# Optimization experiments

Measured on AMD Instinct MI355X. Metric: run time of the kernel, lower is better.

Reference implementation:

```python
import jax, jax.numpy as jnp
import numpy as np

N = 100_000
E = 1_600_000
D_IN, D_H, D_L = 128, 64, 32


def _glorot(key, shape):
    fan_in, fan_out = shape[0], shape[1]
    s = jnp.sqrt(6.0 / (fan_in + fan_out)).astype(jnp.float32)
    return jax.random.uniform(key, shape, jnp.float32, -s, s)


def setup_inputs() -> dict:
    key = jax.random.key(0)
    ks = jax.random.split(key, 8)
    x = jax.random.normal(ks[0], (N, D_IN), jnp.float32)
    edge_index = jax.random.randint(ks[1], (2, E), 0, N, dtype=jnp.int64)
    return {
        "x": x,
        "edge_index": edge_index,
        "W1": _glorot(ks[2], (D_IN, D_H)),
        "b1": jnp.zeros((D_H,), jnp.float32),
        "W2": _glorot(ks[3], (D_H, D_L)),
        "b2": jnp.zeros((D_L,), jnp.float32),
        "Wd1": _glorot(ks[4], (D_L, D_H)),
        "bd1": jnp.zeros((D_H,), jnp.float32),
        "Wd2": _glorot(ks[5], (D_H, D_IN)),
        "bd2": jnp.zeros((D_IN,), jnp.float32),
    }


def gcn_conv(x, W, b, src, dst, num_nodes):
    """PyG GCNConv: add self-loops, symmetric normalization, aggregate, bias."""
    loop = jnp.arange(num_nodes, dtype=src.dtype)
    s = jnp.concatenate([src, loop])  # sources (message senders)
    d = jnp.concatenate([dst, loop])  # targets (message receivers)
    deg = jax.ops.segment_sum(jnp.ones_like(s, dtype=x.dtype), d, num_segments=num_nodes)
    dinv = jnp.where(deg > 0, jax.lax.rsqrt(deg), 0.0)
    norm = dinv[s] * dinv[d]                      # [E+N]
    h = x @ W                                     # [N, out] dense transform first
    msgs = h[s] * norm[:, None]                   # gather + scale, [E+N, out]
    out = jax.ops.segment_sum(msgs, d, num_segments=num_nodes)  # scatter-add
    return out + b


def reference(x, edge_index, W1, b1, W2, b2, Wd1, bd1, Wd2, bd2):
    src, dst = edge_index[0], edge_index[1]
    n = x.shape[0]
    z = gcn_conv(x, W1, b1, src, dst, n)
    z = jax.nn.relu(z)
    z = gcn_conv(z, W2, b2, src, dst, n)          # latent embedding
    h = jax.nn.relu(z @ Wd1 + bd1)
    reconstructed_x = h @ Wd2 + bd2
    return (reconstructed_x, z)
```

## Files before the change

### kernel.cpp

```cpp
#include <hip/hip_runtime.h>
#include <stdint.h>

#define N_NODES 100000
#define N_EDGES 1600000
#define D_INF   128
#define D_HID   64
#define D_LAT   32
#define NB      98

typedef __attribute__((ext_vector_type(8))) short bf16x8;
typedef __attribute__((ext_vector_type(4))) float f32x4;
typedef __attribute__((ext_vector_type(8))) unsigned short u16x8;

__device__ __forceinline__ unsigned short f2bf(float v) {
  union { float f; unsigned int u; } x; x.f = v;
  unsigned int u = x.u + 0x7FFF + ((x.u >> 16) & 1);
  return (unsigned short)(u >> 16);
}
__device__ __forceinline__ float bf2f(unsigned short h) {
  union { unsigned int u; float f; } x; x.u = ((unsigned int)h) << 16;
  return x.f;
}


#define NBKT      196
#define BKT_SHIFT 9
#define BKT_CAP   10240
#define EPB       4096
#define ABLOCKS   391
#define SPLITB    4
#define SPLITC    4

__global__ void k_zeroinit(int* __restrict__ counts, int* __restrict__ bkcnt) {
  int i = blockIdx.x * 256 + threadIdx.x;
  if (i < N_NODES) counts[i] = 0;
  if (blockIdx.x == 0 && threadIdx.x < NBKT) bkcnt[threadIdx.x] = 0;
}

__global__ __launch_bounds__(256) void k_binA(const int* __restrict__ esrc,
                                              const int* __restrict__ edst,
                                              int* __restrict__ bkcnt,
                                              int2* __restrict__ stage) {
  __shared__ int cnt[NBKT];
  __shared__ int sc[256];
  __shared__ int garel[NBKT];
  __shared__ int pos[NBKT];
  __shared__ __align__(16) int2 stg[EPB];
  __shared__ int gaddr[EPB];
  int t = threadIdx.x;
  int e0 = blockIdx.x * EPB;

  for (int i = t; i < NBKT; i += 256) cnt[i] = 0;
  __syncthreads();

  int ds[16], ss[16];
  const int4* s4 = (const int4*)esrc;
  const int4* d4 = (const int4*)edst;
#pragma unroll
  for (int i = 0; i < 4; i++) {
    int idx4 = (e0 >> 2) + i * 256 + t;
    int4 dd = make_int4(-1, -1, -1, -1);
    int4 sv = make_int4(0, 0, 0, 0);
    if (idx4 < N_EDGES / 4) { dd = d4[idx4]; sv = s4[idx4]; }
    ds[i*4+0] = dd.x; ds[i*4+1] = dd.y; ds[i*4+2] = dd.z; ds[i*4+3] = dd.w;
    ss[i*4+0] = sv.x; ss[i*4+1] = sv.y; ss[i*4+2] = sv.z; ss[i*4+3] = sv.w;
  }
#pragma unroll
  for (int j = 0; j < 16; j++)
    if (ds[j] >= 0) atomicAdd(&cnt[ds[j] >> BKT_SHIFT], 1);
  __syncthreads();

  int c = (t < NBKT) ? cnt[t] : 0;
  sc[t] = c;
  __syncthreads();
  int incl = c;
#pragma unroll
  for (int off = 1; off < 256; off <<= 1) {
    int x = (t >= off) ? sc[t - off] : 0;
    __syncthreads();
    incl += x;
    sc[t] = incl;
    __syncthreads();
  }
  if (t < NBKT) {
    int lb = incl - c;
    int gb = 0;
    if (c > 0) gb = t * BKT_CAP + atomicAdd(&bkcnt[t], c);
    garel[t] = gb - lb;
    pos[t]   = lb;
  }
  __syncthreads();

#pragma unroll
  for (int j = 0; j < 16; j++) {
    if (ds[j] >= 0) {
      int b  = ds[j] >> BKT_SHIFT;
      int lp = atomicAdd(&pos[b], 1);
      stg[lp]   = make_int2(ss[j], ds[j]);
      gaddr[lp] = garel[b] + lp;
    }
  }
  __syncthreads();

  int nval = N_EDGES - e0; if (nval > EPB) nval = EPB;
  for (int i = t; i < nval; i += 256)
    stage[gaddr[i]] = stg[i];
}

__global__ __launch_bounds__(256) void k_countB(const int2* __restrict__ stage,
                                                const int* __restrict__ bkcnt,
                                                int* __restrict__ counts) {
  __shared__ int hist[1 << BKT_SHIFT];
  int b   = blockIdx.x / SPLITC;
  int sub = blockIdx.x % SPLITC;
  int t = threadIdx.x;
  for (int i = t; i < (1 << BKT_SHIFT); i += 256) hist[i] = 0;
  __syncthreads();
  int n = bkcnt[b];
  int nlo = b << BKT_SHIFT;
  const int2* reg = stage + (size_t)b * BKT_CAP;
  for (int i = sub * 256 + t; i < n; i += SPLITC * 256)
    atomicAdd(&hist[reg[i].y - nlo], 1);
  __syncthreads();
  for (int i = t; i < (1 << BKT_SHIFT); i += 256) {
    int node = nlo + i;
    if (node < N_NODES) {
      int v = hist[i];
      if (v) atomicAdd(&counts[node], v);
    }
  }
}

__global__ void k_blocksum(const int* __restrict__ counts, int* __restrict__ bsums) {
  __shared__ int red[4];
  int base = blockIdx.x * 1024 + threadIdx.x * 4;
  int s = 0;
#pragma unroll
  for (int j = 0; j < 4; j++) { int i = base + j; if (i < N_NODES) s += counts[i]; }
#pragma unroll
  for (int off = 32; off > 0; off >>= 1) s += __shfl_down(s, off, 64);
  if ((threadIdx.x & 63) == 0) red[threadIdx.x >> 6] = s;
  __syncthreads();
  if (threadIdx.x == 0) bsums[blockIdx.x] = red[0] + red[1] + red[2] + red[3];
}

__global__ void k_scanblocks(const int* __restrict__ bsums, int* __restrict__ bbase,
                             int* __restrict__ offsets) {
  __shared__ int sh[128];
  int t = threadIdx.x;
  int v = (t < NB) ? bsums[t] : 0;
  sh[t] = v;
  __syncthreads();
  int incl = v;
#pragma unroll
  for (int off = 1; off < 128; off <<= 1) {
    int x = (t >= off) ? sh[t - off] : 0;
    __syncthreads();
    incl += x;
    sh[t] = incl;
    __syncthreads();
  }
  if (t < NB) bbase[t] = incl - v;
  if (t == NB - 1) offsets[N_NODES] = incl;
}

__global__ void k_scanchunk(const int* __restrict__ counts, const int* __restrict__ bbase,
                            int* __restrict__ offsets, int* __restrict__ cursor,
                            float* __restrict__ dinv) {
  __shared__ int sh[256];
  int b = blockIdx.x, t = threadIdx.x;
  int base = b * 1024 + t * 4;
  int v[4]; int s = 0;
#pragma unroll
  for (int j = 0; j < 4; j++) { v[j] = (base + j < N_NODES) ? counts[base + j] : 0; s += v[j]; }
  sh[t] = s;
  __syncthreads();
  int incl = s;
#pragma unroll
  for (int off = 1; off < 256; off <<= 1) {
    int x = (t >= off) ? sh[t - off] : 0;
    __syncthreads();
    incl += x;
    sh[t] = incl;
    __syncthreads();
  }
  int run = bbase[b] + incl - s;
#pragma unroll
  for (int j = 0; j < 4; j++) {
    int i = base + j;
    if (i < N_NODES) {
      offsets[i] = run;
      cursor[i]  = run;
      dinv[i]    = rsqrtf((float)(v[j] + 1));
      run += v[j];
    }
  }
}

__global__ __launch_bounds__(256) void k_binB(const int2* __restrict__ stage,
                                              const int* __restrict__ bkcnt,
                                              int* __restrict__ cursor,
                                              const float* __restrict__ dinv,
                                              int2* __restrict__ csr8) {
  int b   = blockIdx.x / SPLITB;
  int sub = blockIdx.x % SPLITB;
  int n = bkcnt[b];
  const int2* reg = stage + (size_t)b * BKT_CAP;
  for (int i = sub * 256 + threadIdx.x; i < n; i += SPLITB * 256) {
    int2 e = reg[i];
    int slot = atomicAdd(&cursor[e.y], 1);
    float w = dinv[e.x] * dinv[e.y];
    csr8[slot] = make_int2(e.x, __float_as_int(w));
  }
}


__global__ void k_prep_w(const float* __restrict__ W1, const float* __restrict__ W2,
                         const float* __restrict__ Wd1, const float* __restrict__ Wd2,
                         unsigned short* __restrict__ w1hi, unsigned short* __restrict__ w1lo,
                         unsigned short* __restrict__ w2hi, unsigned short* __restrict__ w2lo,
                         unsigned short* __restrict__ wd1hi, unsigned short* __restrict__ wd1lo,
                         unsigned short* __restrict__ wd2hi, unsigned short* __restrict__ wd2lo) {
  const float* src; unsigned short *hi, *lo; int K, M;
  switch (blockIdx.x) {
    case 0:  src = W1;  hi = w1hi;  lo = w1lo;  K = 128; M = 64;  break;
    case 1:  src = W2;  hi = w2hi;  lo = w2lo;  K = 64;  M = 32;  break;
    case 2:  src = Wd1; hi = wd1hi; lo = wd1lo; K = 32;  M = 64;  break;
    default: src = Wd2; hi = wd2hi; lo = wd2lo; K = 64;  M = 128; break;
  }
  int KP = K + 8;
  for (int i = threadIdx.x; i < K * M; i += 256) {
    int k = i / M, c = i % M;
    float v = src[i];
    unsigned short h = f2bf(v);
    hi[c * KP + k] = h;
    lo[c * KP + k] = f2bf(v - bf2f(h));
  }
}


template<int NODES, int K, int M>
__global__ __launch_bounds__(256) void k_mfma_gemm(const float* __restrict__ X,
                                                   const unsigned short* __restrict__ Bhi,
                                                   const unsigned short* __restrict__ Blo,
                                                   unsigned short* __restrict__ Y16) {
  constexpr int KP     = K + 8;
  constexpr int NSTRIP = M / 16;
  constexpr int KSTEPS = K / 32;
  constexpr int MTW    = (NODES / 16) * NSTRIP / 4;
  __shared__ __align__(16) unsigned short Ahi[NODES * KP];
  __shared__ __align__(16) unsigned short Alo[NODES * KP];

  int t = threadIdx.x;
  int node0 = blockIdx.x * NODES;

  for (int i = t; i < NODES * K / 4; i += 256) {
    int n = i / (K / 4), f4 = i % (K / 4);
    float4 v = make_float4(0.f, 0.f, 0.f, 0.f);
    if (node0 + n < N_NODES) v = ((const float4*)(X + (size_t)(node0 + n) * K))[f4];
    int base = n * KP + f4 * 4;
    float vv[4] = {v.x, v.y, v.z, v.w};
#pragma unroll
    for (int j = 0; j < 4; j++) {
      unsigned short h = f2bf(vv[j]);
      Ahi[base + j] = h;
      Alo[base + j] = f2bf(vv[j] - bf2f(h));
    }
  }
  __syncthreads();

  int w = t >> 6, lane = t & 63;
  int quad = lane >> 4, r16 = lane & 15;
  int strip = w % NSTRIP;

  bf16x8 bh[KSTEPS], bl[KSTEPS];
  const unsigned short* bp = Bhi + (strip * 16 + r16) * KP + quad * 8;
  const unsigned short* bq = Blo + (strip * 16 + r16) * KP + quad * 8;
#pragma unroll
  for (int ks = 0; ks < KSTEPS; ks++) {
    bh[ks] = *(const bf16x8*)(bp + ks * 32);
    bl[ks] = *(const bf16x8*)(bq + ks * 32);
  }

#pragma unroll
  for (int c = 0; c < MTW; c++) {
    int mt = (w / NSTRIP) * MTW + c;
    f32x4 acc = {0.f, 0.f, 0.f, 0.f};
    const unsigned short* ap = &Ahi[(mt * 16 + r16) * KP + quad * 8];
    const unsigned short* aq = &Alo[(mt * 16 + r16) * KP + quad * 8];
#pragma unroll
    for (int ks = 0; ks < KSTEPS; ks++) {
      bf16x8 ah = *(const bf16x8*)(ap + ks * 32);
      bf16x8 al = *(const bf16x8*)(aq + ks * 32);
      acc = __builtin_amdgcn_mfma_f32_16x16x32_bf16(ah, bh[ks], acc, 0, 0, 0);
      acc = __builtin_amdgcn_mfma_f32_16x16x32_bf16(ah, bl[ks], acc, 0, 0, 0);
      acc = __builtin_amdgcn_mfma_f32_16x16x32_bf16(al, bh[ks], acc, 0, 0, 0);
    }
    int gn  = node0 + mt * 16 + quad * 4;
    int col = strip * 16 + r16;
#pragma unroll
    for (int r = 0; r < 4; r++) {
      if (gn + r < N_NODES) Y16[(size_t)(gn + r) * M + col] = f2bf(acc[r]);
    }
  }
}


template<int FEAT, bool RELU>
__global__ __launch_bounds__(256) void k_aggregate(const unsigned short* __restrict__ H16,
                            const int* __restrict__ offsets,
                            const int2* __restrict__ csr8,
                            const float* __restrict__ dinv, const float* __restrict__ bias,
                            float* __restrict__ OUT) {
  constexpr int LPE    = FEAT / 8;
  constexpr int GROUPS = 64 / LPE;

  int node = blockIdx.x * 4 + (threadIdx.x >> 6);
  int lane = threadIdx.x & 63;
  if (node >= N_NODES) return;
  int beg = offsets[node], end = offsets[node + 1];
  int g  = lane / LPE;
  int f8 = lane % LPE;

  float a0=0.f,a1=0.f,a2=0.f,a3=0.f,a4=0.f,a5=0.f,a6=0.f,a7=0.f;

  for (int p = beg; p < end; p += 2 * GROUPS) {
    int q0 = p + g, q1 = p + GROUPS + g;
    int2 e0 = (q0 < end) ? csr8[q0] : make_int2(node, 0);
    int2 e1 = (q1 < end) ? csr8[q1] : make_int2(node, 0);
    u16x8 h0 = *(const u16x8*)(H16 + (size_t)e0.x * FEAT + f8 * 8);
    u16x8 h1 = *(const u16x8*)(H16 + (size_t)e1.x * FEAT + f8 * 8);
    float w0 = __int_as_float(e0.y), w1 = __int_as_float(e1.y);
    a0 += bf2f(h0[0]) * w0; a1 += bf2f(h0[1]) * w0;
    a2 += bf2f(h0[2]) * w0; a3 += bf2f(h0[3]) * w0;
    a4 += bf2f(h0[4]) * w0; a5 += bf2f(h0[5]) * w0;
    a6 += bf2f(h0[6]) * w0; a7 += bf2f(h0[7]) * w0;
    a0 += bf2f(h1[0]) * w1; a1 += bf2f(h1[1]) * w1;
    a2 += bf2f(h1[2]) * w1; a3 += bf2f(h1[3]) * w1;
    a4 += bf2f(h1[4]) * w1; a5 += bf2f(h1[5]) * w1;
    a6 += bf2f(h1[6]) * w1; a7 += bf2f(h1[7]) * w1;
  }

#pragma unroll
  for (int off = LPE; off < 64; off <<= 1) {
    a0 += __shfl_xor(a0, off, 64);
    a1 += __shfl_xor(a1, off, 64);
    a2 += __shfl_xor(a2, off, 64);
    a3 += __shfl_xor(a3, off, 64);
    a4 += __shfl_xor(a4, off, 64);
    a5 += __shfl_xor(a5, off, 64);
    a6 += __shfl_xor(a6, off, 64);
    a7 += __shfl_xor(a7, off, 64);
  }

  if (g == 0) {
    float di = dinv[node];
    float sw = di * di;
    u16x8 hs = *(const u16x8*)(H16 + (size_t)node * FEAT + f8 * 8);
    float4 bv0 = *(const float4*)(bias + f8 * 8);
    float4 bv1 = *(const float4*)(bias + f8 * 8 + 4);
    a0 += bf2f(hs[0]) * sw + bv0.x;
    a1 += bf2f(hs[1]) * sw + bv0.y;
    a2 += bf2f(hs[2]) * sw + bv0.z;
    a3 += bf2f(hs[3]) * sw + bv0.w;
    a4 += bf2f(hs[4]) * sw + bv1.x;
    a5 += bf2f(hs[5]) * sw + bv1.y;
    a6 += bf2f(hs[6]) * sw + bv1.z;
    a7 += bf2f(hs[7]) * sw + bv1.w;
    if (RELU) {
      a0 = fmaxf(a0, 0.f); a1 = fmaxf(a1, 0.f);
      a2 = fmaxf(a2, 0.f); a3 = fmaxf(a3, 0.f);
      a4 = fmaxf(a4, 0.f); a5 = fmaxf(a5, 0.f);
      a6 = fmaxf(a6, 0.f); a7 = fmaxf(a7, 0.f);
    }
    float4 o0; o0.x = a0; o0.y = a1; o0.z = a2; o0.w = a3;
    float4 o1; o1.x = a4; o1.y = a5; o1.z = a6; o1.w = a7;
    *(float4*)(OUT + (size_t)node * FEAT + f8 * 8)     = o0;
    *(float4*)(OUT + (size_t)node * FEAT + f8 * 8 + 4) = o1;
  }
}


__global__ __launch_bounds__(256) void k_decoder_mfma(
    const float* __restrict__ Z,
    const unsigned short* __restrict__ B1hi, const unsigned short* __restrict__ B1lo,
    const float* __restrict__ bd1,
    const unsigned short* __restrict__ B2hi, const unsigned short* __restrict__ B2lo,
    const float* __restrict__ bd2, float* __restrict__ RECON) {
  constexpr int KP1 = 40;
  constexpr int KP2 = 72;
  __shared__ __align__(16) unsigned short Azhi[64 * KP1];
  __shared__ __align__(16) unsigned short Azlo[64 * KP1];
  __shared__ __align__(16) unsigned short H3hi[64 * KP2];
  __shared__ __align__(16) unsigned short H3lo[64 * KP2];
  int t = threadIdx.x;
  int node0 = blockIdx.x * 64;

  for (int i = t; i < 512; i += 256) {
    int n = i >> 3, f4 = i & 7;
    float4 v = make_float4(0.f, 0.f, 0.f, 0.f);
    if (node0 + n < N_NODES) v = ((const float4*)(Z + (size_t)(node0 + n) * 32))[f4];
    int base = n * KP1 + f4 * 4;
    float vv[4] = {v.x, v.y, v.z, v.w};
#pragma unroll
    for (int j = 0; j < 4; j++) {
      unsigned short h = f2bf(vv[j]);
      Azhi[base + j] = h;
      Azlo[base + j] = f2bf(vv[j] - bf2f(h));
    }
  }
  __syncthreads();

  int w = t >> 6, lane = t & 63;
  int quad = lane >> 4, r16 = lane & 15;

  {
    int col = w * 16 + r16;
    float bias1 = bd1[col];
    bf16x8 bh = *(const bf16x8*)(B1hi + col * KP1 + quad * 8);
    bf16x8 bl = *(const bf16x8*)(B1lo + col * KP1 + quad * 8);
#pragma unroll
    for (int m = 0; m < 4; m++) {
      bf16x8 ah = *(const bf16x8*)(Azhi + (m * 16 + r16) * KP1 + quad * 8);
      bf16x8 al = *(const bf16x8*)(Azlo + (m * 16 + r16) * KP1 + quad * 8);
      f32x4 acc = {0.f, 0.f, 0.f, 0.f};
      acc = __builtin_amdgcn_mfma_f32_16x16x32_bf16(ah, bh, acc, 0, 0, 0);
      acc = __builtin_amdgcn_mfma_f32_16x16x32_bf16(ah, bl, acc, 0, 0, 0);
      acc = __builtin_amdgcn_mfma_f32_16x16x32_bf16(al, bh, acc, 0, 0, 0);
#pragma unroll
      for (int r = 0; r < 4; r++) {
        int row = m * 16 + quad * 4 + r;
        float hv = fmaxf(acc[r] + bias1, 0.f);
        unsigned short h = f2bf(hv);
        H3hi[row * KP2 + col] = h;
        H3lo[row * KP2 + col] = f2bf(hv - bf2f(h));
      }
    }
  }
  __syncthreads();

#pragma unroll
  for (int sp = 0; sp < 2; sp++) {
    int strip = w + sp * 4;
    int col = strip * 16 + r16;
    float bias2 = bd2[col];
    const unsigned short* b2h = B2hi + col * KP2 + quad * 8;
    const unsigned short* b2l = B2lo + col * KP2 + quad * 8;
    bf16x8 bh0 = *(const bf16x8*)(b2h);
    bf16x8 bh1 = *(const bf16x8*)(b2h + 32);
    bf16x8 bl0 = *(const bf16x8*)(b2l);
    bf16x8 bl1 = *(const bf16x8*)(b2l + 32);
#pragma unroll
    for (int m = 0; m < 4; m++) {
      const unsigned short* ahp = H3hi + (m * 16 + r16) * KP2 + quad * 8;
      const unsigned short* alp = H3lo + (m * 16 + r16) * KP2 + quad * 8;
      bf16x8 ah0 = *(const bf16x8*)(ahp);
      bf16x8 ah1 = *(const bf16x8*)(ahp + 32);
      bf16x8 al0 = *(const bf16x8*)(alp);
      bf16x8 al1 = *(const bf16x8*)(alp + 32);
      f32x4 acc = {0.f, 0.f, 0.f, 0.f};
      acc = __builtin_amdgcn_mfma_f32_16x16x32_bf16(ah0, bh0, acc, 0, 0, 0);
      acc = __builtin_amdgcn_mfma_f32_16x16x32_bf16(ah1, bh1, acc, 0, 0, 0);
      acc = __builtin_amdgcn_mfma_f32_16x16x32_bf16(ah0, bl0, acc, 0, 0, 0);
      acc = __builtin_amdgcn_mfma_f32_16x16x32_bf16(ah1, bl1, acc, 0, 0, 0);
      acc = __builtin_amdgcn_mfma_f32_16x16x32_bf16(al0, bh0, acc, 0, 0, 0);
      acc = __builtin_amdgcn_mfma_f32_16x16x32_bf16(al1, bh1, acc, 0, 0, 0);
#pragma unroll
      for (int r = 0; r < 4; r++) {
        int n = node0 + m * 16 + quad * 4 + r;
        if (n < N_NODES) RECON[(size_t)n * 128 + col] = acc[r] + bias2;
      }
    }
  }
}


extern "C" void kernel_launch(void* const* d_in, const int* in_sizes, int n_in,
                              void* d_out, int out_size, void* d_ws, size_t ws_size,
                              hipStream_t stream) {
  const float* x    = (const float*)d_in[0];
  const int*   eidx = (const int*)d_in[1];
  const int*   esrc = eidx;
  const int*   edst = eidx + N_EDGES;
  const float* W1  = (const float*)d_in[2];
  const float* b1  = (const float*)d_in[3];
  const float* W2  = (const float*)d_in[4];
  const float* b2  = (const float*)d_in[5];
  const float* Wd1 = (const float*)d_in[6];
  const float* bd1 = (const float*)d_in[7];
  const float* Wd2 = (const float*)d_in[8];
  const float* bd2 = (const float*)d_in[9];

  float* recon = (float*)d_out;
  float* z     = (float*)d_out + (size_t)N_NODES * D_INF;
  int2*           stage = (int2*)recon;
  unsigned short* h1_16 = (unsigned short*)recon;
  float*          z1    = (float*)((char*)recon + 12800000);
  unsigned short* h2_16 = (unsigned short*)((char*)recon + 38400000);

  char* ws = (char*)d_ws;
  int*   counts  = (int*)(ws + 0);
  int*   offsets = (int*)(ws + 409600);
  int*   cursor  = (int*)(ws + 819200);
  float* dinv    = (float*)(ws + 1228800);
  int*   bsums   = (int*)(ws + 1638400);
  int*   bbase   = (int*)(ws + 1639424);
  int2*  csr8    = (int2*)(ws + 1640448);
  unsigned short* w1hi  = (unsigned short*)(ws + 14440448);
  unsigned short* w1lo  = (unsigned short*)(ws + 14457856);
  unsigned short* w2hi  = (unsigned short*)(ws + 14475264);
  unsigned short* w2lo  = (unsigned short*)(ws + 14479872);
  unsigned short* wd1hi = (unsigned short*)(ws + 14484480);
  unsigned short* wd1lo = (unsigned short*)(ws + 14489600);
  unsigned short* wd2hi = (unsigned short*)(ws + 14494720);
  unsigned short* wd2lo = (unsigned short*)(ws + 14513152);
  int*   bkcnt  = (int*)(ws + 14531584);

  k_zeroinit<<<391, 256, 0, stream>>>(counts, bkcnt);
  k_binA<<<ABLOCKS, 256, 0, stream>>>(esrc, edst, bkcnt, stage);
  k_countB<<<NBKT * SPLITC, 256, 0, stream>>>(stage, bkcnt, counts);
  k_blocksum<<<NB, 256, 0, stream>>>(counts, bsums);
  k_scanblocks<<<1, 128, 0, stream>>>(bsums, bbase, offsets);
  k_scanchunk<<<NB, 256, 0, stream>>>(counts, bbase, offsets, cursor, dinv);
  k_binB<<<NBKT * SPLITB, 256, 0, stream>>>(stage, bkcnt, cursor, dinv, csr8);
  k_prep_w<<<4, 256, 0, stream>>>(W1, W2, Wd1, Wd2, w1hi, w1lo, w2hi, w2lo,
                                  wd1hi, wd1lo, wd2hi, wd2lo);

  k_mfma_gemm<64, 128, 64><<<(N_NODES + 63) / 64, 256, 0, stream>>>(x, w1hi, w1lo, h1_16);
  k_aggregate<64, true><<<(N_NODES + 3) / 4, 256, 0, stream>>>(h1_16, offsets, csr8, dinv, b1, z1);
  k_mfma_gemm<64, 64, 32><<<(N_NODES + 63) / 64, 256, 0, stream>>>(z1, w2hi, w2lo, h2_16);
  k_aggregate<32, false><<<(N_NODES + 3) / 4, 256, 0, stream>>>(h2_16, offsets, csr8, dinv, b2, z);
  k_decoder_mfma<<<(N_NODES + 63) / 64, 256, 0, stream>>>(z, wd1hi, wd1lo, bd1,
                                                          wd2hi, wd2lo, bd2, recon);
}
```

Baseline: 324.7 us.

## Build per-bucket CSR in one kernel and fold degree normalization into GEMM

Replaces the global count/scan/scatter pipeline (countB, blocksum, two scans, binB with global atomics) with a single per-bucket kernel that builds a local histogram, scan and CSR inside each 512-node bucket, storing begin/count per node and 4-byte source indices. The symmetric normalization is refactored so the GEMM epilogue pre-scales rows by dinv[src] and the aggregate applies dinv[dst] once at the end, removing per-edge weights from the CSR. binA also drops its gaddr staging array. The aim is fewer launches, no global atomics on cursors, and half the edge bytes read during aggregation. The cost is a bucket-padded CSR layout and a change in bf16 rounding order.

```diff
diff --git a/kernel.cpp b/kernel.cpp
--- a/kernel.cpp
+++ b/kernel.cpp
@@ -6,7 +6,6 @@
 #define D_INF   128
 #define D_HID   64
 #define D_LAT   32
-#define NB      98
 
 typedef __attribute__((ext_vector_type(8))) short bf16x8;
 typedef __attribute__((ext_vector_type(4))) float f32x4;
@@ -28,13 +27,9 @@
 #define BKT_CAP   10240
 #define EPB       4096
 #define ABLOCKS   391
-#define SPLITB    4
-#define SPLITC    4
-
-__global__ void k_zeroinit(int* __restrict__ counts, int* __restrict__ bkcnt) {
-  int i = blockIdx.x * 256 + threadIdx.x;
-  if (i < N_NODES) counts[i] = 0;
-  if (blockIdx.x == 0 && threadIdx.x < NBKT) bkcnt[threadIdx.x] = 0;
+
+__global__ void k_zerobkt(int* __restrict__ bkcnt) {
+  if (threadIdx.x < NBKT) bkcnt[threadIdx.x] = 0;
 }
 
 __global__ __launch_bounds__(256) void k_binA(const int* __restrict__ esrc,
@@ -46,7 +41,6 @@
   __shared__ int garel[NBKT];
   __shared__ int pos[NBKT];
   __shared__ __align__(16) int2 stg[EPB];
-  __shared__ int gaddr[EPB];
   int t = threadIdx.x;
   int e0 = blockIdx.x * EPB;
 
@@ -96,121 +90,61 @@
     if (ds[j] >= 0) {
       int b  = ds[j] >> BKT_SHIFT;
       int lp = atomicAdd(&pos[b], 1);
-      stg[lp]   = make_int2(ss[j], ds[j]);
-      gaddr[lp] = garel[b] + lp;
+      stg[lp] = make_int2(ss[j], ds[j]);
     }
   }
   __syncthreads();
 
   int nval = N_EDGES - e0; if (nval > EPB) nval = EPB;
-  for (int i = t; i < nval; i += 256)
-    stage[gaddr[i]] = stg[i];
-}
-
-__global__ __launch_bounds__(256) void k_countB(const int2* __restrict__ stage,
-                                                const int* __restrict__ bkcnt,
-                                                int* __restrict__ counts) {
-  __shared__ int hist[1 << BKT_SHIFT];
-  int b   = blockIdx.x / SPLITC;
-  int sub = blockIdx.x % SPLITC;
-  int t = threadIdx.x;
-  for (int i = t; i < (1 << BKT_SHIFT); i += 256) hist[i] = 0;
+  for (int i = t; i < nval; i += 256) {
+    int2 e = stg[i];
+    stage[garel[e.y >> BKT_SHIFT] + i] = e;
+  }
+}
+
+__global__ __launch_bounds__(512) void k_csr(const int2* __restrict__ stage,
+                                             const int* __restrict__ bkcnt,
+                                             int* __restrict__ beg,
+                                             int* __restrict__ cnt,
+                                             float* __restrict__ dinv,
+                                             int* __restrict__ csr4) {
+  __shared__ int hist[512];
+  __shared__ int scan[512];
+  int b = blockIdx.x, t = threadIdx.x;
+  hist[t] = 0;
   __syncthreads();
   int n = bkcnt[b];
   int nlo = b << BKT_SHIFT;
   const int2* reg = stage + (size_t)b * BKT_CAP;
-  for (int i = sub * 256 + t; i < n; i += SPLITC * 256)
+  for (int i = t; i < n; i += 512)
     atomicAdd(&hist[reg[i].y - nlo], 1);
   __syncthreads();
-  for (int i = t; i < (1 << BKT_SHIFT); i += 256) {
-    int node = nlo + i;
-    if (node < N_NODES) {
-      int v = hist[i];
-      if (v) atomicAdd(&counts[node], v);
-    }
-  }
-}
-
-__global__ void k_blocksum(const int* __restrict__ counts, int* __restrict__ bsums) {
-  __shared__ int red[4];
-  int base = blockIdx.x * 1024 + threadIdx.x * 4;
-  int s = 0;
-#pragma unroll
-  for (int j = 0; j < 4; j++) { int i = base + j; if (i < N_NODES) s += counts[i]; }
-#pragma unroll
-  for (int off = 32; off > 0; off >>= 1) s += __shfl_down(s, off, 64);
-  if ((threadIdx.x & 63) == 0) red[threadIdx.x >> 6] = s;
-  __syncthreads();
-  if (threadIdx.x == 0) bsums[blockIdx.x] = red[0] + red[1] + red[2] + red[3];
-}
-
-__global__ void k_scanblocks(const int* __restrict__ bsums, int* __restrict__ bbase,
-                             int* __restrict__ offsets) {
-  __shared__ int sh[128];
-  int t = threadIdx.x;
-  int v = (t < NB) ? bsums[t] : 0;
-  sh[t] = v;
+  int v = hist[t];
+  scan[t] = v;
   __syncthreads();
   int incl = v;
 #pragma unroll
-  for (int off = 1; off < 128; off <<= 1) {
-    int x = (t >= off) ? sh[t - off] : 0;
+  for (int off = 1; off < 512; off <<= 1) {
+    int x = (t >= off) ? scan[t - off] : 0;
     __syncthreads();
     incl += x;
-    sh[t] = incl;
+    scan[t] = incl;
     __syncthreads();
   }
-  if (t < NB) bbase[t] = incl - v;
-  if (t == NB - 1) offsets[N_NODES] = incl;
-}
-
-__global__ void k_scanchunk(const int* __restrict__ counts, const int* __restrict__ bbase,
-                            int* __restrict__ offsets, int* __restrict__ cursor,
-                            float* __restrict__ dinv) {
-  __shared__ int sh[256];
-  int b = blockIdx.x, t = threadIdx.x;
-  int base = b * 1024 + t * 4;
-  int v[4]; int s = 0;
-#pragma unroll
-  for (int j = 0; j < 4; j++) { v[j] = (base + j < N_NODES) ? counts[base + j] : 0; s += v[j]; }
-  sh[t] = s;
-  __syncthreads();
-  int incl = s;
-#pragma unroll
-  for (int off = 1; off < 256; off <<= 1) {
-    int x = (t >= off) ? sh[t - off] : 0;
-    __syncthreads();
-    incl += x;
-    sh[t] = incl;
-    __syncthreads();
-  }
-  int run = bbase[b] + incl - s;
-#pragma unroll
-  for (int j = 0; j < 4; j++) {
-    int i = base + j;
-    if (i < N_NODES) {
-      offsets[i] = run;
-      cursor[i]  = run;
-      dinv[i]    = rsqrtf((float)(v[j] + 1));
-      run += v[j];
-    }
-  }
-}
-
-__global__ __launch_bounds__(256) void k_binB(const int2* __restrict__ stage,
-                                              const int* __restrict__ bkcnt,
-                                              int* __restrict__ cursor,
-                                              const float* __restrict__ dinv,
-                                              int2* __restrict__ csr8) {
-  int b   = blockIdx.x / SPLITB;
-  int sub = blockIdx.x % SPLITB;
-  int n = bkcnt[b];
-  const int2* reg = stage + (size_t)b * BKT_CAP;
-  for (int i = sub * 256 + threadIdx.x; i < n; i += SPLITB * 256) {
+  int loc = incl - v;
+  int node = nlo + t;
+  if (node < N_NODES) {
+    beg[node]  = b * BKT_CAP + loc;
+    cnt[node]  = v;
+    dinv[node] = rsqrtf((float)(v + 1));
+  }
+  scan[t] = loc;
+  __syncthreads();
+  int* c4 = csr4 + (size_t)b * BKT_CAP;
+  for (int i = t; i < n; i += 512) {
     int2 e = reg[i];
-    int slot = atomicAdd(&cursor[e.y], 1);
-    float w = dinv[e.x] * dinv[e.y];
-    csr8[slot] = make_int2(e.x, __float_as_int(w));
+    int slot = atomicAdd(&scan[e.y - nlo], 1);
+    c4[slot] = e.x;
   }
 }
 
@@ -243,6 +177,7 @@
 __global__ __launch_bounds__(256) void k_mfma_gemm(const float* __restrict__ X,
                                                    const unsigned short* __restrict__ Bhi,
                                                    const unsigned short* __restrict__ Blo,
+                                                   const float* __restrict__ dinv,
                                                    unsigned short* __restrict__ Y16) {
   constexpr int KP     = K + 8;
   constexpr int NSTRIP = M / 16;
@@ -300,7 +235,8 @@
     int col = strip * 16 + r16;
 #pragma unroll
     for (int r = 0; r < 4; r++) {
-      if (gn + r < N_NODES) Y16[(size_t)(gn + r) * M + col] = f2bf(acc[r]);
+      if (gn + r < N_NODES)
+        Y16[(size_t)(gn + r) * M + col] = f2bf(acc[r] * dinv[gn + r]);
     }
   }
 }
@@ -308,8 +244,9 @@
 
 template<int FEAT, bool RELU>
 __global__ __launch_bounds__(256) void k_aggregate(const unsigned short* __restrict__ H16,
-                            const int* __restrict__ offsets,
-                            const int2* __restrict__ csr8,
+                            const int* __restrict__ beg,
+                            const int* __restrict__ cnt,
+                            const int* __restrict__ csr4,
                             const float* __restrict__ dinv, const float* __restrict__ bias,
                             float* __restrict__ OUT) {
   constexpr int LPE    = FEAT / 8;
@@ -318,27 +255,28 @@
   int node = blockIdx.x * 4 + (threadIdx.x >> 6);
   int lane = threadIdx.x & 63;
   if (node >= N_NODES) return;
-  int beg = offsets[node], end = offsets[node + 1];
+  int bg = beg[node], end = bg + cnt[node];
   int g  = lane / LPE;
   int f8 = lane % LPE;
 
   float a0=0.f,a1=0.f,a2=0.f,a3=0.f,a4=0.f,a5=0.f,a6=0.f,a7=0.f;
 
-  for (int p = beg; p < end; p += 2 * GROUPS) {
+  for (int p = bg; p < end; p += 2 * GROUPS) {
     int q0 = p + g, q1 = p + GROUPS + g;
-    int2 e0 = (q0 < end) ? csr8[q0] : make_int2(node, 0);
-    int2 e1 = (q1 < end) ? csr8[q1] : make_int2(node, 0);
-    u16x8 h0 = *(const u16x8*)(H16 + (size_t)e0.x * FEAT + f8 * 8);
-    u16x8 h1 = *(const u16x8*)(H16 + (size_t)e1.x * FEAT + f8 * 8);
-    float w0 = __int_as_float(e0.y), w1 = __int_as_float(e1.y);
-    a0 += bf2f(h0[0]) * w0; a1 += bf2f(h0[1]) * w0;
-    a2 += bf2f(h0[2]) * w0; a3 += bf2f(h0[3]) * w0;
-    a4 += bf2f(h0[4]) * w0; a5 += bf2f(h0[5]) * w0;
-    a6 += bf2f(h0[6]) * w0; a7 += bf2f(h0[7]) * w0;
-    a0 += bf2f(h1[0]) * w1; a1 += bf2f(h1[1]) * w1;
-    a2 += bf2f(h1[2]) * w1; a3 += bf2f(h1[3]) * w1;
-    a4 += bf2f(h1[4]) * w1; a5 += bf2f(h1[5]) * w1;
-    a6 += bf2f(h1[6]) * w1; a7 += bf2f(h1[7]) * w1;
+    int s0 = (q0 < end) ? csr4[q0] : node;
+    int s1 = (q1 < end) ? csr4[q1] : node;
+    float m0 = (q0 < end) ? 1.f : 0.f;
+    float m1 = (q1 < end) ? 1.f : 0.f;
+    u16x8 h0 = *(const u16x8*)(H16 + (size_t)s0 * FEAT + f8 * 8);
+    u16x8 h1 = *(const u16x8*)(H16 + (size_t)s1 * FEAT + f8 * 8);
+    a0 += bf2f(h0[0]) * m0; a1 += bf2f(h0[1]) * m0;
+    a2 += bf2f(h0[2]) * m0; a3 += bf2f(h0[3]) * m0;
+    a4 += bf2f(h0[4]) * m0; a5 += bf2f(h0[5]) * m0;
+    a6 += bf2f(h0[6]) * m0; a7 += bf2f(h0[7]) * m0;
+    a0 += bf2f(h1[0]) * m1; a1 += bf2f(h1[1]) * m1;
+    a2 += bf2f(h1[2]) * m1; a3 += bf2f(h1[3]) * m1;
+    a4 += bf2f(h1[4]) * m1; a5 += bf2f(h1[5]) * m1;
+    a6 += bf2f(h1[6]) * m1; a7 += bf2f(h1[7]) * m1;
   }
 
 #pragma unroll
@@ -355,18 +293,17 @@
 
   if (g == 0) {
     float di = dinv[node];
-    float sw = di * di;
     u16x8 hs = *(const u16x8*)(H16 + (size_t)node * FEAT + f8 * 8);
     float4 bv0 = *(const float4*)(bias + f8 * 8);
     float4 bv1 = *(const float4*)(bias + f8 * 8 + 4);
-    a0 += bf2f(hs[0]) * sw + bv0.x;
-    a1 += bf2f(hs[1]) * sw + bv0.y;
-    a2 += bf2f(hs[2]) * sw + bv0.z;
-    a3 += bf2f(hs[3]) * sw + bv0.w;
-    a4 += bf2f(hs[4]) * sw + bv1.x;
-    a5 += bf2f(hs[5]) * sw + bv1.y;
-    a6 += bf2f(hs[6]) * sw + bv1.z;
-    a7 += bf2f(hs[7]) * sw + bv1.w;
+    a0 = (a0 + bf2f(hs[0])) * di + bv0.x;
+    a1 = (a1 + bf2f(hs[1])) * di + bv0.y;
+    a2 = (a2 + bf2f(hs[2])) * di + bv0.z;
+    a3 = (a3 + bf2f(hs[3])) * di + bv0.w;
+    a4 = (a4 + bf2f(hs[4])) * di + bv1.x;
+    a5 = (a5 + bf2f(hs[5])) * di + bv1.y;
+    a6 = (a6 + bf2f(hs[6])) * di + bv1.z;
+    a7 = (a7 + bf2f(hs[7])) * di + bv1.w;
     if (RELU) {
       a0 = fmaxf(a0, 0.f); a1 = fmaxf(a1, 0.f);
       a2 = fmaxf(a2, 0.f); a3 = fmaxf(a3, 0.f);
@@ -499,37 +436,30 @@
   unsigned short* h2_16 = (unsigned short*)((char*)recon + 38400000);
 
   char* ws = (char*)d_ws;
-  int*   counts  = (int*)(ws + 0);
-  int*   offsets = (int*)(ws + 409600);
-  int*   cursor  = (int*)(ws + 819200);
-  float* dinv    = (float*)(ws + 1228800);
-  int*   bsums   = (int*)(ws + 1638400);
-  int*   bbase   = (int*)(ws + 1639424);
-  int2*  csr8    = (int2*)(ws + 1640448);
-  unsigned short* w1hi  = (unsigned short*)(ws + 14440448);
-  unsigned short* w1lo  = (unsigned short*)(ws + 14457856);
-  unsigned short* w2hi  = (unsigned short*)(ws + 14475264);
-  unsigned short* w2lo  = (unsigned short*)(ws + 14479872);
-  unsigned short* wd1hi = (unsigned short*)(ws + 14484480);
-  unsigned short* wd1lo = (unsigned short*)(ws + 14489600);
-  unsigned short* wd2hi = (unsigned short*)(ws + 14494720);
-  unsigned short* wd2lo = (unsigned short*)(ws + 14513152);
-  int*   bkcnt  = (int*)(ws + 14531584);
-
-  k_zeroinit<<<391, 256, 0, stream>>>(counts, bkcnt);
+  int*   beg    = (int*)(ws + 0);
+  int*   cntn   = (int*)(ws + 409600);
+  float* dinv   = (float*)(ws + 819200);
+  int*   bkcnt  = (int*)(ws + 1228800);
+  int*   csr4   = (int*)(ws + 1229824);
+  unsigned short* w1hi  = (unsigned short*)(ws + 9257984);
+  unsigned short* w1lo  = (unsigned short*)(ws + 9275392);
+  unsigned short* w2hi  = (unsigned short*)(ws + 9292800);
+  unsigned short* w2lo  = (unsigned short*)(ws + 9297408);
+  unsigned short* wd1hi = (unsigned short*)(ws + 9302016);
+  unsigned short* wd1lo = (unsigned short*)(ws + 9307136);
+  unsigned short* wd2hi = (unsigned short*)(ws + 9312256);
+  unsigned short* wd2lo = (unsigned short*)(ws + 9330688);
+
+  k_zerobkt<<<1, 256, 0, stream>>>(bkcnt);
   k_binA<<<ABLOCKS, 256, 0, stream>>>(esrc, edst, bkcnt, stage);
-  k_countB<<<NBKT * SPLITC, 256, 0, stream>>>(stage, bkcnt, counts);
-  k_blocksum<<<NB, 256, 0, stream>>>(counts, bsums);
-  k_scanblocks<<<1, 128, 0, stream>>>(bsums, bbase, offsets);
-  k_scanchunk<<<NB, 256, 0, stream>>>(counts, bbase, offsets, cursor, dinv);
-  k_binB<<<NBKT * SPLITB, 256, 0, stream>>>(stage, bkcnt, cursor, dinv, csr8);
+  k_csr<<<NBKT, 512, 0, stream>>>(stage, bkcnt, beg, cntn, dinv, csr4);
   k_prep_w<<<4, 256, 0, stream>>>(W1, W2, Wd1, Wd2, w1hi, w1lo, w2hi, w2lo,
                                   wd1hi, wd1lo, wd2hi, wd2lo);
 
-  k_mfma_gemm<64, 128, 64><<<(N_NODES + 63) / 64, 256, 0, stream>>>(x, w1hi, w1lo, h1_16);
-  k_aggregate<64, true><<<(N_NODES + 3) / 4, 256, 0, stream>>>(h1_16, offsets, csr8, dinv, b1, z1);
-  k_mfma_gemm<64, 64, 32><<<(N_NODES + 63) / 64, 256, 0, stream>>>(z1, w2hi, w2lo, h2_16);
-  k_aggregate<32, false><<<(N_NODES + 3) / 4, 256, 0, stream>>>(h2_16, offsets, csr8, dinv, b2, z);
+  k_mfma_gemm<64, 128, 64><<<(N_NODES + 63) / 64, 256, 0, stream>>>(x, w1hi, w1lo, dinv, h1_16);
+  k_aggregate<64, true><<<(N_NODES + 3) / 4, 256, 0, stream>>>(h1_16, beg, cntn, csr4, dinv, b1, z1);
+  k_mfma_gemm<64, 64, 32><<<(N_NODES + 63) / 64, 256, 0, stream>>>(z1, w2hi, w2lo, dinv, h2_16);
+  k_aggregate<32, false><<<(N_NODES + 3) / 4, 256, 0, stream>>>(h2_16, beg, cntn, csr4, dinv, b2, z);
   k_decoder_mfma<<<(N_NODES + 63) / 64, 256, 0, stream>>>(z, wd1hi, wd1lo, bd1,
                                                           wd2hi, wd2lo, bd2, recon);
 }
```

Result: faster. 290.0 us (-10.7%).
